# Performance work log

Measured on AMD Instinct MI355X. Metric: run time of the kernel, lower is better.

Reference implementation:

```python
import jax, jax.numpy as jnp
import numpy as np

NUM_HEADS = 12


def setup_inputs() -> dict:
    key = jax.random.key(0)
    k1, k2, k3, k4 = jax.random.split(key, 4)
    B, N, C = 32, 577, 768
    x = jax.random.normal(k1, (B, N, C), dtype=jnp.float32)
    qkv_w = jax.random.normal(k2, (3 * C, C), dtype=jnp.float32) * 0.02
    proj_w = jax.random.normal(k3, (C, C), dtype=jnp.float32) * 0.02
    proj_b = jax.random.normal(k4, (C,), dtype=jnp.float32) * 0.02
    return {"x": x, "qkv_w": qkv_w, "proj_w": proj_w, "proj_b": proj_b,
            "reduction_num": 115}


def reference(x, qkv_w, proj_w, proj_b, reduction_num):
    B, N, C = x.shape
    H = NUM_HEADS
    hd = C // H
    scale = hd ** -0.5

    # qkv projection (no bias), split into q, k, v of shape (B, H, N, hd)
    qkv = (x @ qkv_w.T).reshape(B, N, 3, H, hd)
    qkv = jnp.transpose(qkv, (2, 0, 3, 1, 4))  # (3, B, H, N, hd)
    q, k, v = qkv[0], qkv[1], qkv[2]

    attn = jax.nn.softmax(jnp.einsum('bhnd,bhmd->bhnm', q * scale, k), axis=-1)  # (B,H,N,N)

    # diagonal entries at positions 1..N-1 (skip CLS), averaged over heads
    attn_diag = jnp.diagonal(attn, axis1=-2, axis2=-1)[:, :, 1:].mean(axis=1)  # (B, N-1)

    token_rank = jnp.argsort(-attn_diag, axis=1)  # descending
    num_kept = N - reduction_num
    kept = token_rank[:, : N - 1 - reduction_num] + 1  # token indices (non-CLS)
    index_cls = jnp.zeros((B, 1), dtype=kept.dtype)
    index_kept = jnp.sort(jnp.concatenate([index_cls, kept], axis=1), axis=1)  # (B, num_kept)

    # gather kept query rows of the attention matrix: (B, H, num_kept, N)
    weight = jnp.take_along_axis(attn, index_kept[:, None, :, None], axis=2)

    out = jnp.einsum('bhkn,bhnd->bhkd', weight, v)  # (B, H, num_kept, hd)
    out = jnp.transpose(out, (0, 2, 1, 3)).reshape(B, num_kept, C)
    out = out @ proj_w.T + proj_b

    original_x = jnp.take_along_axis(x, index_kept[:, :, None], axis=1)  # (B, num_kept, C)
    return out + original_x
```

## Files before the change

kernel.cpp:

```cpp
#include <hip/hip_runtime.h>
#include <math.h>

#define BB_   32
#define NN_   577
#define CC_   768
#define HH_   12
#define HD_   64
#define NPAD  640
#define BH_   (BB_*HH_)
#define MQ    (BB_*NN_)
#define KEPT  462
#define KEPTP 464
#define MP    (BB_*KEPT)
#define TOPK  461

#define MT_   145
#define NT_   18

using short8 = __attribute__((ext_vector_type(8))) short;
using f32x4  = __attribute__((ext_vector_type(4))) float;
using u16x4  = __attribute__((ext_vector_type(4))) unsigned short;
using u32x2  = __attribute__((ext_vector_type(2))) unsigned int;

using gp1_t = const __attribute__((address_space(1))) void*;
using sp3_t = __attribute__((address_space(3))) void*;

__device__ __forceinline__ unsigned short f2bf(float f) {
  unsigned int u = __float_as_uint(f);
  u += 0x7fffu + ((u >> 16) & 1u);
  return (unsigned short)(u >> 16);
}
__device__ __forceinline__ float bf2f(unsigned short h) {
  return __uint_as_float(((unsigned int)h) << 16);
}
__device__ __forceinline__ f32x4 mfma16(short8 a, short8 b, f32x4 c) {
  return __builtin_amdgcn_mfma_f32_16x16x32_bf16(a, b, c, 0, 0, 0);
}
__device__ __forceinline__ void gl_lds16(const void* g, void* l) {
  __builtin_amdgcn_global_load_lds((gp1_t)g, (sp3_t)l, 16, 0, 0);
}

#define SC_ 0.18033688011112042f

__device__ __forceinline__ void split4(const float* __restrict__ in, int i,
                                       unsigned short* __restrict__ hi,
                                       unsigned short* __restrict__ lo) {
  f32x4 f = *(const f32x4*)(in + (size_t)i * 4);
  u16x4 hv, lv;
#pragma unroll
  for (int j = 0; j < 4; ++j) {
    unsigned short h = f2bf(f[j]);
    hv[j] = h;
    lv[j] = f2bf(f[j] - bf2f(h));
  }
  *(u16x4*)(hi + (size_t)i * 4) = hv;
  if (lo) *(u16x4*)(lo + (size_t)i * 4) = lv;
}

#define NX4_ (MQ * 768 / 4)
#define NW4_ (2304 * 768 / 4)
#define NP4_ (768 * 768 / 4)

__global__ __launch_bounds__(256) void k_split_all(
    const float* __restrict__ x, const float* __restrict__ qw,
    const float* __restrict__ pw,
    unsigned short* __restrict__ xh, unsigned short* __restrict__ xl,
    unsigned short* __restrict__ wh, unsigned short* __restrict__ wl,
    unsigned short* __restrict__ pwh) {
  int i2 = blockIdx.x * 256 + threadIdx.x;
#pragma unroll
  for (int s = 0; s < 2; ++s) {
    int i = 2 * i2 + s;
    if (i < NX4_) {
      split4(x, i, xh, xl);
    } else if (i < NX4_ + NW4_) {
      split4(qw, i - NX4_, wh, wl);
    } else if (i < NX4_ + NW4_ + NP4_) {
      split4(pw, i - NX4_ - NW4_, pwh, (unsigned short*)nullptr);
    }
  }
}

__global__ __launch_bounds__(256, 2) void k_qkv(
    const unsigned short* __restrict__ xh, const unsigned short* __restrict__ xl,
    const unsigned short* __restrict__ wh, const unsigned short* __restrict__ wl,
    unsigned short* __restrict__ qh, unsigned short* __restrict__ ql,
    unsigned short* __restrict__ kh, unsigned short* __restrict__ kl,
    unsigned short* __restrict__ vt) {
  __shared__ char smem[65536];
  unsigned short* lAh = (unsigned short*)smem;
  unsigned short* lAl = (unsigned short*)(smem + 16384);
  unsigned short* lBh = (unsigned short*)(smem + 32768);
  unsigned short* lBl = (unsigned short*)(smem + 49152);

  const int tid = threadIdx.x;
  const int wave = tid >> 6, lane = tid & 63, lr = lane & 15, lg = lane >> 4;
  const int wm = wave >> 1, wn = wave & 1;

  const int nwg = MT_ * NT_;
  const int qq = nwg >> 3, rr = nwg & 7;
  int orig = blockIdx.x;
  int xcd = orig & 7, pos = orig >> 3;
  int wgid = (xcd < rr ? xcd * (qq + 1) : rr * (qq + 1) + (xcd - rr) * qq) + pos;
  const int mt = wgid / NT_, nt = wgid - mt * NT_;
  const int m0 = mt * 128, n0 = nt * 128;
  const int which = n0 / 768;
  const bool three = (which < 2);

  f32x4 zf = {0.f, 0.f, 0.f, 0.f};
  f32x4 acc[4][4];
#pragma unroll
  for (int a = 0; a < 4; ++a)
#pragma unroll
    for (int bq = 0; bq < 4; ++bq) acc[a][bq] = zf;

  for (int ks = 0; ks < 12; ++ks) {
    const int k0 = ks * 64;
#pragma unroll
    for (int it = 0; it < 4; ++it) {
      int c = it * 256 + tid;
      int row = c >> 3, slot = c & 7;
      int grow = m0 + row; if (grow > MQ - 1) grow = MQ - 1;
      int gk = k0 + ((slot ^ (row & 7)) << 3);
      gl_lds16(xh + (size_t)grow * 768 + gk,
               (char*)lAh + (it * 256 + wave * 64) * 16);
      if (three)
        gl_lds16(xl + (size_t)grow * 768 + gk,
                 (char*)lAl + (it * 256 + wave * 64) * 16);
    }
#pragma unroll
    for (int it = 0; it < 4; ++it) {
      int c = it * 256 + tid;
      int row = c >> 3, slot = c & 7;
      int gn = n0 + row;
      int gk = k0 + ((slot ^ (row & 7)) << 3);
      gl_lds16(wh + (size_t)gn * 768 + gk,
               (char*)lBh + (it * 256 + wave * 64) * 16);
      if (three)
        gl_lds16(wl + (size_t)gn * 768 + gk,
                 (char*)lBl + (it * 256 + wave * 64) * 16);
    }
    __syncthreads();

#pragma unroll
    for (int kk = 0; kk < 2; ++kk) {
      short8 fa[4], fal[4], fb[4], fbl[4];
#pragma unroll
      for (int ms = 0; ms < 4; ++ms) {
        int row = wm * 64 + ms * 16 + lr;
        int off = (kk * 64 + lg * 16) ^ ((row & 7) << 4);
        fa[ms] = *(const short8*)((const char*)lAh + row * 128 + off);
        if (three) fal[ms] = *(const short8*)((const char*)lAl + row * 128 + off);
      }
#pragma unroll
      for (int ns = 0; ns < 4; ++ns) {
        int row = wn * 64 + ns * 16 + lr;
        int off = (kk * 64 + lg * 16) ^ ((row & 7) << 4);
        fb[ns] = *(const short8*)((const char*)lBh + row * 128 + off);
        if (three) fbl[ns] = *(const short8*)((const char*)lBl + row * 128 + off);
      }
#pragma unroll
      for (int ms = 0; ms < 4; ++ms)
#pragma unroll
        for (int ns = 0; ns < 4; ++ns) {
          acc[ms][ns] = mfma16(fa[ms], fb[ns], acc[ms][ns]);
          if (three) {
            acc[ms][ns] = mfma16(fa[ms], fbl[ns], acc[ms][ns]);
            acc[ms][ns] = mfma16(fal[ms], fb[ns], acc[ms][ns]);
          }
        }
    }
    __syncthreads();
  }

  if (which < 2) {
    float* lC = (float*)smem;
    for (int p = 0; p < 2; ++p) {
      if (p) __syncthreads();
      if (wn == p) {
#pragma unroll
        for (int ms = 0; ms < 4; ++ms)
#pragma unroll
          for (int ns = 0; ns < 4; ++ns) {
            int r = wm * 64 + ms * 16 + 4 * lg;
            int cc = ns * 16 + lr;
#pragma unroll
            for (int reg = 0; reg < 4; ++reg)
              lC[(r + reg) * 66 + cc] = acc[ms][ns][reg];
          }
      }
      __syncthreads();
      const int h = ((n0 % 768) >> 6) + p;
      int r = tid >> 1, c0 = (tid & 1) * 32;
      int m = m0 + r;
      if (m < MQ) {
        int b = m / 577, n = m % 577;
        size_t base = ((size_t)(b * 12 + h) * NPAD + n) * 64 + c0;
        unsigned short* dh = (which == 0 ? qh : kh) + base;
        unsigned short* dl = (which == 0 ? ql : kl) + base;
#pragma unroll
        for (int cc = 0; cc < 32; cc += 4) {
          u16x4 hv, lv;
#pragma unroll
          for (int j = 0; j < 4; ++j) {
            float f = lC[r * 66 + c0 + cc + j];
            unsigned short hh = f2bf(f);
            hv[j] = hh;
            lv[j] = f2bf(f - bf2f(hh));
          }
          *(u16x4*)(dh + cc) = hv;
          *(u16x4*)(dl + cc) = lv;
        }
      }
    }
  } else {
    const int h0 = (n0 % 768) >> 6;
#pragma unroll
    for (int ms = 0; ms < 4; ++ms)
#pragma unroll
      for (int ns = 0; ns < 4; ++ns) {
        int m = m0 + wm * 64 + ms * 16 + 4 * lg;
        int c = wn * 64 + ns * 16 + lr;
        int h = h0 + (c >> 6), d = c & 63;
        int b = m / 577, n = m - b * 577;
        if (m + 3 < MQ && n + 3 < 577) {
          u16x4 pv;
#pragma unroll
          for (int reg = 0; reg < 4; ++reg) pv[reg] = f2bf(acc[ms][ns][reg]);
          *(u16x4*)(vt + ((size_t)(b * 12 + h) * 64 + d) * NPAD + n) = pv;
        } else {
#pragma unroll
          for (int reg = 0; reg < 4; ++reg) {
            int mm = m + reg;
            if (mm < MQ) {
              int bb = mm / 577, nn = mm - bb * 577;
              vt[((size_t)(bb * 12 + h) * 64 + d) * NPAD + nn] = f2bf(acc[ms][ns][reg]);
            }
          }
        }
      }
  }
}

__global__ __launch_bounds__(256) void k_attn1(
    const unsigned short* __restrict__ qh, const unsigned short* __restrict__ ql,
    const unsigned short* __restrict__ kh, const unsigned short* __restrict__ kl,
    const unsigned short* __restrict__ vt, float* __restrict__ S0,
    float* __restrict__ Dg, unsigned short* __restrict__ Ob) {
  __shared__ char smem[45056];
  char* lK = smem;
  char* lV = smem + 16384;
  char* lP = smem + 24576;

  int wgid = (blockIdx.x & 7) * 240 + (blockIdx.x >> 3);
  const int bh = wgid / 5;
  const int i0 = (wgid - bh * 5) * 128;
  const int tid = threadIdx.x, w = tid >> 6, lane = tid & 63;
  const int lr = lane & 15, lg = lane >> 4;
  const size_t qb = (size_t)bh * NPAD * 64;

  const int krow = tid >> 3, kslot = tid & 7;
  const int vrow = tid >> 2, vslot = tid & 3;
  const size_t ksrc = (size_t)krow * 64 + ((kslot ^ (krow & 7)) << 3);
  const size_t vsrc = ((size_t)bh * 64 + vrow) * NPAD + ((vslot ^ (vrow & 3)) << 3);

  short8 qf[2][2], qfl[2][2];
#pragma unroll
  for (int iu = 0; iu < 2; ++iu) {
    const size_t qrow = qb + (size_t)(i0 + w * 32 + iu * 16 + lr) * 64;
#pragma unroll
    for (int kk = 0; kk < 2; ++kk) {
      qf[iu][kk]  = *(const short8*)(qh + qrow + kk * 32 + lg * 8);
      qfl[iu][kk] = *(const short8*)(ql + qrow + kk * 32 + lg * 8);
    }
  }
  f32x4 zf = {0.f, 0.f, 0.f, 0.f};
  f32x4 oacc[2][4];
#pragma unroll
  for (int iu = 0; iu < 2; ++iu)
#pragma unroll
    for (int ds = 0; ds < 4; ++ds) oacc[iu][ds] = zf;
  float s0[2] = {0.0f, 0.0f};

  gl_lds16(kh + qb + ksrc, lK + tid * 16);
  gl_lds16(kl + qb + ksrc, lK + 4096 + tid * 16);
  gl_lds16(vt + vsrc, lV + tid * 16);
  __syncthreads();

  int buf = 0, pb = 0;
  char* lPw = lP + w * 5120;
  for (int jp = 0; jp < 19; ++jp) {
    if (jp < 18) {
      int jn = (jp + 1) * 32;
      gl_lds16(kh + qb + (size_t)jn * 64 + ksrc, lK + (buf ^ 1) * 8192 + tid * 16);
      gl_lds16(kl + qb + (size_t)jn * 64 + ksrc, lK + (buf ^ 1) * 8192 + 4096 + tid * 16);
      gl_lds16(vt + vsrc + jn, lV + (buf ^ 1) * 4096 + tid * 16);
    }
#pragma unroll
    for (int t = 0; t < 2; ++t) {
      const int jloc = t * 16 + lr;
      short8 kfh[2], kfl2[2];
#pragma unroll
      for (int kk = 0; kk < 2; ++kk) {
        int off = (kk * 64 + lg * 16) ^ ((jloc & 7) << 4);
        kfh[kk]  = *(const short8*)(lK + buf * 8192 + jloc * 128 + off);
        kfl2[kk] = *(const short8*)(lK + buf * 8192 + 4096 + jloc * 128 + off);
      }
      int jbase = jp * 32 + t * 16 + 4 * lg;
#pragma unroll
      for (int iu = 0; iu < 2; ++iu) {
        f32x4 c = zf;
#pragma unroll
        for (int kk = 0; kk < 2; ++kk) {
          c = mfma16(kfh[kk], qfl[iu][kk], c);
          c = mfma16(kfl2[kk], qf[iu][kk], c);
          c = mfma16(kfh[kk], qf[iu][kk], c);
        }
        float p0 = (jbase + 0 < 577) ? exp2f(c[0] * SC_) : 0.0f;
        float p1 = (jbase + 1 < 577) ? exp2f(c[1] * SC_) : 0.0f;
        float p2 = (jbase + 2 < 577) ? exp2f(c[2] * SC_) : 0.0f;
        float p3 = (jbase + 3 < 577) ? exp2f(c[3] * SC_) : 0.0f;
        s0[iu] += (p0 + p1) + (p2 + p3);
        u32x2 wv;
        wv[0] = (unsigned)f2bf(p0) | ((unsigned)f2bf(p1) << 16);
        wv[1] = (unsigned)f2bf(p2) | ((unsigned)f2bf(p3) << 16);
        *(u32x2*)(lPw + iu * 2560 + pb * 1280 + lr * 80 + t * 32 + lg * 8) = wv;
      }
    }
    asm volatile("" ::: "memory");
#pragma unroll
    for (int iu = 0; iu < 2; ++iu) {
      short8 pa = *(const short8*)(lPw + iu * 2560 + pb * 1280 + lr * 80 + lg * 16);
#pragma unroll
      for (int ds = 0; ds < 4; ++ds) {
        int r = ds * 16 + lr;
        int off = (lg * 16) ^ ((r & 3) << 4);
        short8 vf = *(const short8*)(lV + buf * 4096 + r * 64 + off);
        oacc[iu][ds] = mfma16(pa, vf, oacc[iu][ds]);
      }
    }
    asm volatile("" ::: "memory");
    pb ^= 1;
    __syncthreads();
    buf ^= 1;
  }

#pragma unroll
  for (int iu = 0; iu < 2; ++iu) {
    float s = s0[iu];
    s += __shfl_xor(s, 16);
    s += __shfl_xor(s, 32);
    const int iw = i0 + w * 32 + iu * 16;
    if (lg == 0) S0[(size_t)bh * NPAD + iw + lr] = s;
    float rs[4];
#pragma unroll
    for (int reg = 0; reg < 4; ++reg) rs[reg] = 1.0f / __shfl(s, 4 * lg + reg);
#pragma unroll
    for (int ds = 0; ds < 4; ++ds)
#pragma unroll
      for (int reg = 0; reg < 4; ++reg)
        Ob[((size_t)bh * NPAD + iw + 4 * lg + reg) * 64 + ds * 16 + lr] =
            f2bf(oacc[iu][ds][reg] * rs[reg]);
  }

#pragma unroll
  for (int rr = 0; rr < 2; ++rr) {
    const int row = i0 + rr * 64 + (tid >> 2);
    const int c = tid & 3;
    const size_t base = qb + (size_t)row * 64 + c * 16;
    short8 a0 = *(const short8*)(qh + base), a1 = *(const short8*)(qh + base + 8);
    short8 b0 = *(const short8*)(ql + base), b1 = *(const short8*)(ql + base + 8);
    short8 c0 = *(const short8*)(kh + base), c1 = *(const short8*)(kh + base + 8);
    short8 d0 = *(const short8*)(kl + base), d1 = *(const short8*)(kl + base + 8);
    float acc = 0.0f;
#pragma unroll
    for (int j = 0; j < 8; ++j) {
      float qv = bf2f((unsigned short)a0[j]) + bf2f((unsigned short)b0[j]);
      float kv = bf2f((unsigned short)c0[j]) + bf2f((unsigned short)d0[j]);
      acc += qv * kv;
      float qv1 = bf2f((unsigned short)a1[j]) + bf2f((unsigned short)b1[j]);
      float kv1 = bf2f((unsigned short)c1[j]) + bf2f((unsigned short)d1[j]);
      acc += qv1 * kv1;
    }
    acc += __shfl_xor(acc, 1, 4);
    acc += __shfl_xor(acc, 2, 4);
    if (c == 0) Dg[(size_t)bh * NPAD + row] = acc * SC_;
  }
}

__global__ __launch_bounds__(576) void k_select(const float* __restrict__ Dg,
                                                const float* __restrict__ S0,
                                                int* __restrict__ idxk) {
  __shared__ float kbuf[576];
  __shared__ int kflag[576];
  int b = blockIdx.x, t = threadIdx.x;
  if (t < 576) {
    float a = 0.0f;
#pragma unroll
    for (int h = 0; h < 12; ++h) {
      size_t o = (size_t)(b * 12 + h) * NPAD + t + 1;
      a += exp2f(Dg[o]) / S0[o];
    }
    kbuf[t] = a;
  }
  __syncthreads();
  if (t < 576) {
    float kt = kbuf[t];
    int cnt = 0;
    for (int j = 0; j < 576; ++j) {
      float kj = kbuf[j];
      cnt += (kj > kt || (kj == kt && j < t)) ? 1 : 0;
    }
    kflag[t] = (cnt < TOPK) ? 1 : 0;
  }
  __syncthreads();
  if (t < 576 && kflag[t]) {
    int pos = 1;
    for (int j = 0; j < t; ++j) pos += kflag[j];
    idxk[b * KEPTP + pos] = t + 1;
  }
  if (t == 0) {
    idxk[b * KEPTP + 0] = 0;
    idxk[b * KEPTP + 462] = 0;
    idxk[b * KEPTP + 463] = 0;
  }
}

__global__ __launch_bounds__(256) void k_proj(
    const unsigned short* __restrict__ Ob, const unsigned short* __restrict__ pwh,
    const float* __restrict__ pb, const float* __restrict__ x,
    const int* __restrict__ idxk, float* __restrict__ out) {
  __shared__ char smem[33792];
  unsigned short* lA = (unsigned short*)smem;
  unsigned short* lB = (unsigned short*)(smem + 16384);
  const int tid = threadIdx.x;
  const int wave = tid >> 6, lane = tid & 63, lr = lane & 15, lg = lane >> 4;
  const int wm = wave >> 1, wn = wave & 1;
  int wgid = (blockIdx.x & 7) * 87 + (blockIdx.x >> 3);
  const int mt = wgid / 6, nt = wgid - mt * 6;
  const int m0 = mt * 128, n0 = nt * 128;

  int tokr[4], bbr[4], offr8[4];
#pragma unroll
  for (int it = 0; it < 4; ++it) {
    int c = it * 256 + tid;
    int row = c >> 3, slot = c & 7;
    int m = m0 + row; if (m > MP - 1) m = MP - 1;
    int bb = m / 462, tt = m - bb * 462;
    tokr[it] = idxk[bb * KEPTP + tt];
    bbr[it] = bb;
    offr8[it] = (slot ^ (row & 7)) << 3;
  }

  f32x4 zf = {0.f, 0.f, 0.f, 0.f};
  f32x4 acc[4][4];
#pragma unroll
  for (int a = 0; a < 4; ++a)
#pragma unroll
    for (int bq = 0; bq < 4; ++bq) acc[a][bq] = zf;

  for (int ks = 0; ks < 12; ++ks) {
    int k0 = ks * 64;
#pragma unroll
    for (int it = 0; it < 4; ++it) {
      gl_lds16(Ob + ((size_t)(bbr[it] * 12 + ks) * NPAD + tokr[it]) * 64 + offr8[it],
               (char*)lA + (it * 256 + wave * 64) * 16);
    }
#pragma unroll
    for (int it = 0; it < 4; ++it) {
      int c = it * 256 + tid;
      int row = c >> 3, slot = c & 7;
      int gk = k0 + ((slot ^ (row & 7)) << 3);
      gl_lds16(pwh + (size_t)(n0 + row) * 768 + gk,
               (char*)lB + (it * 256 + wave * 64) * 16);
    }
    __syncthreads();
#pragma unroll
    for (int kk = 0; kk < 2; ++kk) {
      short8 fa[4], fb[4];
#pragma unroll
      for (int ms = 0; ms < 4; ++ms) {
        int row = wm * 64 + ms * 16 + lr;
        int off = (kk * 64 + lg * 16) ^ ((row & 7) << 4);
        fa[ms] = *(const short8*)((const char*)lA + row * 128 + off);
      }
#pragma unroll
      for (int ns = 0; ns < 4; ++ns) {
        int row = wn * 64 + ns * 16 + lr;
        int off = (kk * 64 + lg * 16) ^ ((row & 7) << 4);
        fb[ns] = *(const short8*)((const char*)lB + row * 128 + off);
      }
#pragma unroll
      for (int ms = 0; ms < 4; ++ms)
#pragma unroll
        for (int ns = 0; ns < 4; ++ns)
          acc[ms][ns] = mfma16(fa[ms], fb[ns], acc[ms][ns]);
    }
    __syncthreads();
  }

  float* lC = (float*)smem;
  for (int p = 0; p < 2; ++p) {
    if (p) __syncthreads();
    if (wn == p) {
#pragma unroll
      for (int ms = 0; ms < 4; ++ms)
#pragma unroll
        for (int ns = 0; ns < 4; ++ns) {
          int r = wm * 64 + ms * 16 + 4 * lg;
          int cc = ns * 16 + lr;
#pragma unroll
          for (int reg = 0; reg < 4; ++reg)
            lC[(r + reg) * 66 + cc] = acc[ms][ns][reg];
        }
    }
    __syncthreads();
    int r = tid >> 1, c0 = (tid & 1) * 32;
    int m = m0 + r;
    if (m < MP) {
      int bb = m / 462, tt = m % 462;
      int tok = idxk[bb * KEPTP + tt];
      int col = n0 + p * 64 + c0;
      const float* xs = x + ((size_t)(bb * 577) + tok) * 768 + col;
      float* dst = out + (size_t)m * 768 + col;
#pragma unroll
      for (int cc = 0; cc < 32; cc += 4) {
        f32x4 xv = *(const f32x4*)(xs + cc);
        f32x4 bv = *(const f32x4*)(pb + col + cc);
        f32x4 o;
#pragma unroll
        for (int j = 0; j < 4; ++j)
          o[j] = lC[r * 66 + c0 + cc + j] + bv[j] + xv[j];
        *(f32x4*)(dst + cc) = o;
      }
    }
  }
}

extern "C" void kernel_launch(void* const* d_in, const int* in_sizes, int n_in,
                              void* d_out, int out_size, void* d_ws, size_t ws_size,
                              hipStream_t stream) {
  const float* x  = (const float*)d_in[0];
  const float* qw = (const float*)d_in[1];
  const float* pw = (const float*)d_in[2];
  const float* pb = (const float*)d_in[3];
  (void)in_sizes; (void)n_in; (void)out_size; (void)ws_size;

  char* ws = (char*)d_ws;
  size_t off = 0;
  auto alloc = [&](size_t bytes) {
    void* p = ws + off;
    off += (bytes + 255) & ~(size_t)255;
    return p;
  };
  unsigned short* xh  = (unsigned short*)alloc((size_t)MQ * 768 * 2);
  unsigned short* xl  = (unsigned short*)alloc((size_t)MQ * 768 * 2);
  unsigned short* wh  = (unsigned short*)alloc((size_t)2304 * 768 * 2);
  unsigned short* wl  = (unsigned short*)alloc((size_t)2304 * 768 * 2);
  unsigned short* pwh = (unsigned short*)alloc((size_t)768 * 768 * 2);
  unsigned short* qhp = (unsigned short*)alloc((size_t)BH_ * NPAD * 64 * 2);
  unsigned short* qlp = (unsigned short*)alloc((size_t)BH_ * NPAD * 64 * 2);
  unsigned short* khp = (unsigned short*)alloc((size_t)BH_ * NPAD * 64 * 2);
  unsigned short* klp = (unsigned short*)alloc((size_t)BH_ * NPAD * 64 * 2);
  unsigned short* vtp = (unsigned short*)alloc((size_t)BH_ * NPAD * 64 * 2);
  unsigned short* Obf = (unsigned short*)alloc((size_t)BH_ * NPAD * 64 * 2);
  float* S0  = (float*)alloc((size_t)BH_ * NPAD * 4);
  float* Dg  = (float*)alloc((size_t)BH_ * NPAD * 4);
  int*   idxk = (int*)alloc((size_t)BB_ * KEPTP * 4);

  k_split_all<<<dim3(((NX4_ + NW4_ + NP4_) / 2 + 255) / 256), 256, 0, stream>>>(
      x, qw, pw, xh, xl, wh, wl, pwh);
  k_qkv<<<dim3(MT_ * NT_), 256, 0, stream>>>(xh, xl, wh, wl, qhp, qlp, khp, klp, vtp);
  k_attn1<<<dim3(1920), 256, 0, stream>>>(qhp, qlp, khp, klp, vtp, S0, Dg, Obf);
  k_select<<<dim3(32), 576, 0, stream>>>(Dg, S0, idxk);
  k_proj<<<dim3(696), 256, 0, stream>>>(Obf, pwh, pb, x, idxk, (float*)d_out);
}
```

Baseline: 377.1 us.

## Double-buffer QKV GEMM LDS tiles with K-step halved to overlap loads

Restructures the QKV projection GEMM main loop to use two LDS buffers with a K tile of 32 instead of a single buffer with K tile of 64. The next tile's global-to-LDS loads are issued before computing on the current tile, so memory latency overlaps MFMA work, and there is one barrier per step instead of two. Address precomputation is hoisted out of the loop and the swizzle is changed to match the 64-byte rows. It doubles the number of loop iterations and barriers per K, and overlap depends on whether the direct-to-LDS loads are actually waited on after the compute.

```diff
diff --git a/kernel.cpp b/kernel.cpp
--- a/kernel.cpp
+++ b/kernel.cpp
@@ -88,10 +88,6 @@
     unsigned short* __restrict__ kh, unsigned short* __restrict__ kl,
     unsigned short* __restrict__ vt) {
   __shared__ char smem[65536];
-  unsigned short* lAh = (unsigned short*)smem;
-  unsigned short* lAl = (unsigned short*)(smem + 16384);
-  unsigned short* lBh = (unsigned short*)(smem + 32768);
-  unsigned short* lBl = (unsigned short*)(smem + 49152);
 
   const int tid = threadIdx.x;
   const int wave = tid >> 6, lane = tid & 63, lr = lane & 15, lg = lane >> 4;
@@ -107,6 +103,17 @@
   const int which = n0 / 768;
   const bool three = (which < 2);
 
+  int arow[2], brow[2], goff[2];
+#pragma unroll
+  for (int it = 0; it < 2; ++it) {
+    int c = it * 256 + tid;
+    int row = c >> 2, slot = c & 3;
+    int gr = m0 + row; if (gr > MQ - 1) gr = MQ - 1;
+    arow[it] = gr;
+    brow[it] = n0 + row;
+    goff[it] = (slot ^ (row & 3)) << 3;
+  }
+
   f32x4 zf = {0.f, 0.f, 0.f, 0.f};
   f32x4 acc[4][4];
 #pragma unroll
@@ -114,50 +121,50 @@
 #pragma unroll
     for (int bq = 0; bq < 4; ++bq) acc[a][bq] = zf;
 
-  for (int ks = 0; ks < 12; ++ks) {
-    const int k0 = ks * 64;
-#pragma unroll
-    for (int it = 0; it < 4; ++it) {
-      int c = it * 256 + tid;
-      int row = c >> 3, slot = c & 7;
-      int grow = m0 + row; if (grow > MQ - 1) grow = MQ - 1;
-      int gk = k0 + ((slot ^ (row & 7)) << 3);
-      gl_lds16(xh + (size_t)grow * 768 + gk,
-               (char*)lAh + (it * 256 + wave * 64) * 16);
-      if (three)
-        gl_lds16(xl + (size_t)grow * 768 + gk,
-                 (char*)lAl + (it * 256 + wave * 64) * 16);
-    }
-#pragma unroll
-    for (int it = 0; it < 4; ++it) {
-      int c = it * 256 + tid;
-      int row = c >> 3, slot = c & 7;
-      int gn = n0 + row;
-      int gk = k0 + ((slot ^ (row & 7)) << 3);
-      gl_lds16(wh + (size_t)gn * 768 + gk,
-               (char*)lBh + (it * 256 + wave * 64) * 16);
-      if (three)
-        gl_lds16(wl + (size_t)gn * 768 + gk,
-                 (char*)lBl + (it * 256 + wave * 64) * 16);
-    }
-    __syncthreads();
-
-#pragma unroll
-    for (int kk = 0; kk < 2; ++kk) {
+#pragma unroll
+  for (int it = 0; it < 2; ++it) {
+    int dsto = (it * 256 + tid) * 16;
+    gl_lds16(xh + (size_t)arow[it] * 768 + goff[it], smem + dsto);
+    gl_lds16(wh + (size_t)brow[it] * 768 + goff[it], smem + 16384 + dsto);
+    if (three) {
+      gl_lds16(xl + (size_t)arow[it] * 768 + goff[it], smem + 8192 + dsto);
+      gl_lds16(wl + (size_t)brow[it] * 768 + goff[it], smem + 24576 + dsto);
+    }
+  }
+  __syncthreads();
+
+  int buf = 0;
+  for (int ks = 0; ks < 24; ++ks) {
+    if (ks < 23) {
+      const int kn = (ks + 1) * 32;
+      char* sb = smem + (buf ^ 1) * 32768;
+#pragma unroll
+      for (int it = 0; it < 2; ++it) {
+        int dsto = (it * 256 + tid) * 16;
+        gl_lds16(xh + (size_t)arow[it] * 768 + kn + goff[it], sb + dsto);
+        gl_lds16(wh + (size_t)brow[it] * 768 + kn + goff[it], sb + 16384 + dsto);
+        if (three) {
+          gl_lds16(xl + (size_t)arow[it] * 768 + kn + goff[it], sb + 8192 + dsto);
+          gl_lds16(wl + (size_t)brow[it] * 768 + kn + goff[it], sb + 24576 + dsto);
+        }
+      }
+    }
+    {
+      char* cb = smem + buf * 32768;
       short8 fa[4], fal[4], fb[4], fbl[4];
 #pragma unroll
       for (int ms = 0; ms < 4; ++ms) {
         int row = wm * 64 + ms * 16 + lr;
-        int off = (kk * 64 + lg * 16) ^ ((row & 7) << 4);
-        fa[ms] = *(const short8*)((const char*)lAh + row * 128 + off);
-        if (three) fal[ms] = *(const short8*)((const char*)lAl + row * 128 + off);
+        int off = (lg * 16) ^ ((row & 3) << 4);
+        fa[ms] = *(const short8*)(cb + row * 64 + off);
+        if (three) fal[ms] = *(const short8*)(cb + 8192 + row * 64 + off);
       }
 #pragma unroll
       for (int ns = 0; ns < 4; ++ns) {
         int row = wn * 64 + ns * 16 + lr;
-        int off = (kk * 64 + lg * 16) ^ ((row & 7) << 4);
-        fb[ns] = *(const short8*)((const char*)lBh + row * 128 + off);
-        if (three) fbl[ns] = *(const short8*)((const char*)lBl + row * 128 + off);
+        int off = (lg * 16) ^ ((row & 3) << 4);
+        fb[ns] = *(const short8*)(cb + 16384 + row * 64 + off);
+        if (three) fbl[ns] = *(const short8*)(cb + 24576 + row * 64 + off);
       }
 #pragma unroll
       for (int ms = 0; ms < 4; ++ms)
@@ -170,7 +177,9 @@
           }
         }
     }
+    asm volatile("" ::: "memory");
     __syncthreads();
+    buf ^= 1;
   }
 
   if (which < 2) {
```

New measurement: 381.2 us. No clear change (+1.1%).
